# Kernel tuning notes

Hardware: AMD Instinct MI355X
Metric: run time of the kernel (lower is better)

Reference implementation:

```python
import jax, jax.numpy as jnp
import numpy as np

TIMESCALE = 10.0   # NeuralODE init kwarg
N_MAX = 48         # static upper bound on number of constant-size Dopri5 steps
B, D, H = 8192, 128, 128


def _mlp(y, W1, b1, W2, b2):
    # autonomous dynamics f(x): tanh MLP, applied along last dim
    return jnp.tanh(y @ W1 + b1) @ W2 + b2


def _dopri5_step(y, dt, f):
    # classic Dormand-Prince 5(4) tableau; autonomous f, so c_i unused
    k1 = f(y)
    k2 = f(y + dt * (1.0 / 5.0 * k1))
    k3 = f(y + dt * (3.0 / 40.0 * k1 + 9.0 / 40.0 * k2))
    k4 = f(y + dt * (44.0 / 45.0 * k1 - 56.0 / 15.0 * k2 + 32.0 / 9.0 * k3))
    k5 = f(y + dt * (19372.0 / 6561.0 * k1 - 25360.0 / 2187.0 * k2
                     + 64448.0 / 6561.0 * k3 - 212.0 / 729.0 * k4))
    k6 = f(y + dt * (9017.0 / 3168.0 * k1 - 355.0 / 33.0 * k2
                     + 46732.0 / 5247.0 * k3 + 49.0 / 176.0 * k4
                     - 5103.0 / 18656.0 * k5))
    return y + dt * (35.0 / 384.0 * k1 + 500.0 / 1113.0 * k3
                     + 125.0 / 192.0 * k4 - 2187.0 / 6784.0 * k5
                     + 11.0 / 84.0 * k6)


def _initial_step_size(y0, f0, f, order=4, rtol=1.4e-8, atol=1.4e-8):
    # faithful port of NeuralODE.initial_step_size (Hairer heuristic)
    scale = atol + jnp.abs(y0) * rtol
    d0 = jnp.linalg.norm(y0 / scale)
    d1 = jnp.linalg.norm(f0 / scale)
    h0 = jnp.where((d0 < 1e-5) | (d1 < 1e-5), 1e-6, 0.01 * d0 / d1)
    y1 = y0 + h0 * f0
    f1 = f(y1)
    d2 = jnp.linalg.norm((f1 - f0) / scale) / h0
    h1 = jnp.where((d1 <= 1e-15) & (d2 <= 1e-15),
                   jnp.maximum(1e-6, h0 * 1e-3),
                   (0.01 / (d1 + d2)) ** (1.0 / (order + 1.0)))
    return jnp.minimum(100.0 * h0, h1)


def setup_inputs() -> dict:
    key = jax.random.key(0)
    k0, k1, k2 = jax.random.split(key, 3)
    x = jax.random.normal(k0, (B, D), jnp.float32)
    W1 = jax.random.normal(k1, (D, H), jnp.float32) * (1.0 / D ** 0.5)
    b1 = jnp.zeros((H,), jnp.float32)
    W2 = jax.random.normal(k2, (H, D), jnp.float32) * (1.0 / H ** 0.5)
    b2 = jnp.zeros((D,), jnp.float32)
    t = jnp.ones((1,), jnp.float32)
    return {"t": t, "x": x, "W1": W1, "b1": b1, "W2": W2, "b2": b2}


def reference(t, x, W1, b1, W2, b2):
    f = lambda y: _mlp(y, W1, b1, W2, b2)
    # dt0 from the first state row, exactly as the original (x[0, :])
    dt0 = _initial_step_size(x[0], f(x[0]), f)
    T = t[0] / TIMESCALE  # linspace(0, t/timescale, 2) -> ts = [0, T]

    # diffrax default ConstantStepSize: fixed-dt Dopri5 until t reaches T.
    # Static-length scan with dt clamped to the remaining interval; once
    # t == T, dt == 0 and the step is skipped via lax.cond.
    step = jax.checkpoint(
        lambda y, dt: jax.lax.cond(dt > 0.0,
                                   lambda a: _dopri5_step(a, dt, f),
                                   lambda a: a, y))

    def body(carry, _):
        tt, y = carry
        dt = jnp.clip(T - tt, 0.0, dt0)
        return (tt + dt, step(y, dt)), None

    (_, yT), _ = jax.lax.scan(body, (jnp.zeros((), jnp.float32), x), None,
                              length=N_MAX)
    # SaveAt(ts=[0, T]) -> ys has leading axis n_samples=2
    return jnp.stack([x, yT])
```

## Files before the change

kernel.cpp:

```cpp
#include <hip/hip_runtime.h>


typedef __attribute__((ext_vector_type(8))) short short8;
typedef __attribute__((ext_vector_type(4))) float f32x4;

#define LDSPAD 136

__device__ __forceinline__ short f2bf(float f) {
  union { float f; unsigned u; } v; v.f = f;
  return (short)((v.u + 0x8000u) >> 16);
}

__device__ __forceinline__ float fast_tanh(float x) {
  float e = __expf(2.0f * x);
  return 1.0f - __fdividef(2.0f, e + 1.0f);
}

__global__ __launch_bounds__(256, 2)
void node_kernel(const float* __restrict__ tptr, const float* __restrict__ x,
                 const float* __restrict__ W1, const float* __restrict__ b1,
                 const float* __restrict__ W2, const float* __restrict__ b2,
                 float* __restrict__ out) {
  const int tid  = threadIdx.x;
  const int lane = tid & 63;
  const int wave = tid >> 6;
  const int q    = lane >> 4;
  const int colL = lane & 15;
  const int ctBase = wave * 2;
  const int blockRow = blockIdx.x * 16;

  __shared__ short AbufA[16][LDSPAD];
  __shared__ short AbufB[16][LDSPAD];
  __shared__ float sred[256];
  __shared__ float srowY[128], srowF[128], srowH[128], srowY2[128], srowF2[128], sscale[128];

  short8 w1f[2][4], w2f[2][4];
  float b1c[2], b2c[2];
#pragma unroll
  for (int ci = 0; ci < 2; ++ci) {
    const int n = (ctBase + ci) * 16 + colL;
    b1c[ci] = b1[n];
    b2c[ci] = b2[n];
#pragma unroll
    for (int kt = 0; kt < 4; ++kt) {
      short8 v1, v2;
#pragma unroll
      for (int j = 0; j < 8; ++j) {
        const int k = kt * 32 + q * 8 + j;
        v1[j] = f2bf(W1[k * 128 + n]);
        v2[j] = f2bf(W2[k * 128 + n]);
      }
      w1f[ci][kt] = v1;
      w2f[ci][kt] = v2;
    }
  }

  auto block_sum = [&](float v) -> float {
    sred[tid] = v;
    __syncthreads();
    if (tid < 64) {
      float s = sred[tid] + sred[tid + 64] + sred[tid + 128] + sred[tid + 192];
#pragma unroll
      for (int o = 32; o > 0; o >>= 1) s += __shfl_down(s, o, 64);
      if (tid == 0) sred[0] = s;
    }
    __syncthreads();
    float r = sred[0];
    __syncthreads();
    return r;
  };

  auto mlp_row = [&](const float* yin, float* fout) {
    if (tid < 128) {
      float a = b1[tid];
#pragma unroll 8
      for (int j = 0; j < 128; ++j) a += yin[j] * W1[j * 128 + tid];
      srowH[tid] = fast_tanh(a);
    }
    __syncthreads();
    if (tid < 128) {
      float a = b2[tid];
#pragma unroll 8
      for (int j = 0; j < 128; ++j) a += srowH[j] * W2[j * 128 + tid];
      fout[tid] = a;
    }
    __syncthreads();
  };

  if (tid < 128) srowY[tid] = x[tid];
  __syncthreads();
  mlp_row(srowY, srowF);
  float t0 = 0.f, t1 = 0.f;
  if (tid < 128) {
    float sc = 1.4e-8f + fabsf(srowY[tid]) * 1.4e-8f;
    sscale[tid] = sc;
    float a = srowY[tid] / sc; t0 = a * a;
    float bq = srowF[tid] / sc; t1 = bq * bq;
  }
  float d0 = sqrtf(block_sum(t0));
  float d1 = sqrtf(block_sum(t1));
  float h0 = (d0 < 1e-5f || d1 < 1e-5f) ? 1e-6f : 0.01f * d0 / d1;
  if (tid < 128) srowY2[tid] = srowY[tid] + h0 * srowF[tid];
  __syncthreads();
  mlp_row(srowY2, srowF2);
  float t2 = 0.f;
  if (tid < 128) { float a = (srowF2[tid] - srowF[tid]) / sscale[tid]; t2 = a * a; }
  float d2 = sqrtf(block_sum(t2)) / h0;
  float h1 = (d1 <= 1e-15f && d2 <= 1e-15f) ? fmaxf(1e-6f, h0 * 1e-3f)
                                            : powf(0.01f / (d1 + d2), 0.2f);
  const float dt0v = fminf(100.f * h0, h1);

  float yr[8];
#pragma unroll
  for (int e = 0; e < 8; ++e)
    yr[e] = x[(blockRow + q * 4 + (e & 3)) * 128 + (ctBase + (e >> 2)) * 16 + colL];

  auto stage = [&](const float* v) {
#pragma unroll
    for (int e = 0; e < 8; ++e)
      AbufA[q * 4 + (e & 3)][(ctBase + (e >> 2)) * 16 + colL] = f2bf(v[e]);
    __syncthreads();
  };

  auto evalF = [&](float* kout) {
    f32x4 accH[2];
#pragma unroll
    for (int ci = 0; ci < 2; ++ci) accH[ci] = f32x4{b1c[ci], b1c[ci], b1c[ci], b1c[ci]};
#pragma unroll
    for (int kt = 0; kt < 4; ++kt) {
      short8 a = *(const short8*)&AbufA[colL][kt * 32 + q * 8];
#pragma unroll
      for (int ci = 0; ci < 2; ++ci)
        accH[ci] = __builtin_amdgcn_mfma_f32_16x16x32_bf16(a, w1f[ci][kt], accH[ci], 0, 0, 0);
    }
#pragma unroll
    for (int e = 0; e < 8; ++e)
      AbufB[q * 4 + (e & 3)][(ctBase + (e >> 2)) * 16 + colL] =
          f2bf(fast_tanh(accH[e >> 2][e & 3]));
    __syncthreads();
    f32x4 accF[2];
#pragma unroll
    for (int ci = 0; ci < 2; ++ci) accF[ci] = f32x4{b2c[ci], b2c[ci], b2c[ci], b2c[ci]};
#pragma unroll
    for (int kt = 0; kt < 4; ++kt) {
      short8 a = *(const short8*)&AbufB[colL][kt * 32 + q * 8];
#pragma unroll
      for (int ci = 0; ci < 2; ++ci)
        accF[ci] = __builtin_amdgcn_mfma_f32_16x16x32_bf16(a, w2f[ci][kt], accF[ci], 0, 0, 0);
    }
#pragma unroll
    for (int e = 0; e < 8; ++e) kout[e] = accF[e >> 2][e & 3];
  };

  const float T = tptr[0] / 10.0f;
  float tt = 0.f;
  float k1[8], k2[8], k3[8], k4[8], k5[8], k6[8], yv[8];

#pragma unroll 1
  for (int it = 0; it < 48; ++it) {
    float dt = fminf(fmaxf(T - tt, 0.f), dt0v);
    if (dt > 0.f) {
      stage(yr); evalF(k1);
#pragma unroll
      for (int e = 0; e < 8; ++e) yv[e] = yr[e] + dt * (0.2f * k1[e]);
      stage(yv); evalF(k2);
#pragma unroll
      for (int e = 0; e < 8; ++e) yv[e] = yr[e] + dt * (0.075f * k1[e] + 0.225f * k2[e]);
      stage(yv); evalF(k3);
#pragma unroll
      for (int e = 0; e < 8; ++e)
        yv[e] = yr[e] + dt * (0.9777777777777777f * k1[e] - 3.7333333333333334f * k2[e]
                            + 3.5555555555555554f * k3[e]);
      stage(yv); evalF(k4);
#pragma unroll
      for (int e = 0; e < 8; ++e)
        yv[e] = yr[e] + dt * (2.9525986892242035f * k1[e] - 11.595793324188385f * k2[e]
                            + 9.822892851699436f * k3[e] - 0.2908093278463649f * k4[e]);
      stage(yv); evalF(k5);
#pragma unroll
      for (int e = 0; e < 8; ++e)
        yv[e] = yr[e] + dt * (2.8462752525252526f * k1[e] - 10.757575757575758f * k2[e]
                            + 8.906422717743473f * k3[e] + 0.2784090909090909f * k4[e]
                            - 0.27351165254237287f * k5[e]);
      stage(yv); evalF(k6);
#pragma unroll
      for (int e = 0; e < 8; ++e)
        yr[e] += dt * (0.0911458333333333f * k1[e] + 0.449236298292902f * k3[e]
                     + 0.6510416666666666f * k4[e] - 0.32237617924528303f * k5[e]
                     + 0.13095238095238096f * k6[e]);
    }
    tt += dt;
  }

  {
    const float4* x4 = (const float4*)(x + blockRow * 128);
    float4* o4 = (float4*)(out + blockRow * 128);
#pragma unroll 1
    for (int i = tid; i < 512; i += 256) o4[i] = x4[i];
    float* oy = out + 8192 * 128;
#pragma unroll
    for (int e = 0; e < 8; ++e)
      oy[(blockRow + q * 4 + (e & 3)) * 128 + (ctBase + (e >> 2)) * 16 + colL] = yr[e];
  }
}

extern "C" void kernel_launch(void* const* d_in, const int* in_sizes, int n_in,
                              void* d_out, int out_size, void* d_ws, size_t ws_size,
                              hipStream_t stream) {
  const float* t  = (const float*)d_in[0];
  const float* x  = (const float*)d_in[1];
  const float* W1 = (const float*)d_in[2];
  const float* b1 = (const float*)d_in[3];
  const float* W2 = (const float*)d_in[4];
  const float* b2 = (const float*)d_in[5];
  float* out = (float*)d_out;
  node_kernel<<<dim3(512), dim3(256), 0, stream>>>(t, x, W1, b1, W2, b2, out);
}
```

Baseline: 172.1 us.

## Use 8 waves per block with one column tile each and split prologue MLP

Doubles the block to 512 threads so each wave owns a single 16-column tile instead of two. This halves per-thread weight fragments and accumulators, shortening each wave's serial MFMA chain per stage. The scalar dt0 prologue MLP is split across four K-partitions with a shared-memory partial sum, replacing the single 128-thread dot-product loop. The trade-off is more waves taking part in every __syncthreads barrier and higher per-CU thread pressure at the 512-thread/4-block launch bound.

```diff
diff --git a/kernel.cpp b/kernel.cpp
--- a/kernel.cpp
+++ b/kernel.cpp
@@ -4,7 +4,7 @@
 typedef __attribute__((ext_vector_type(8))) short short8;
 typedef __attribute__((ext_vector_type(4))) float f32x4;
 
-#define LDSPAD 136
+#define SL 136
 
 __device__ __forceinline__ short f2bf(float f) {
   union { float f; unsigned u; } v; v.f = f;
@@ -16,50 +16,46 @@
   return 1.0f - __fdividef(2.0f, e + 1.0f);
 }
 
-__global__ __launch_bounds__(256, 2)
+__global__ __launch_bounds__(512, 4)
 void node_kernel(const float* __restrict__ tptr, const float* __restrict__ x,
                  const float* __restrict__ W1, const float* __restrict__ b1,
                  const float* __restrict__ W2, const float* __restrict__ b2,
                  float* __restrict__ out) {
   const int tid  = threadIdx.x;
   const int lane = tid & 63;
-  const int wave = tid >> 6;
+  const int ct   = tid >> 6;
   const int q    = lane >> 4;
   const int colL = lane & 15;
-  const int ctBase = wave * 2;
+  const int n    = ct * 16 + colL;
   const int blockRow = blockIdx.x * 16;
 
-  __shared__ short AbufA[16][LDSPAD];
-  __shared__ short AbufB[16][LDSPAD];
-  __shared__ float sred[256];
-  __shared__ float srowY[128], srowF[128], srowH[128], srowY2[128], srowF2[128], sscale[128];
+  __shared__ short A1[16][SL];
+  __shared__ short A2[16][SL];
+  __shared__ float sred[512];
+  __shared__ float spart[4][128];
+  __shared__ float srowY[128], srowH[128], srowF[128], srowY2[128], srowF2[128], sscale[128];
 
-  short8 w1f[2][4], w2f[2][4];
-  float b1c[2], b2c[2];
+  short8 w1f[4], w2f[4];
+  const float b1c = b1[n], b2c = b2[n];
 #pragma unroll
-  for (int ci = 0; ci < 2; ++ci) {
-    const int n = (ctBase + ci) * 16 + colL;
-    b1c[ci] = b1[n];
-    b2c[ci] = b2[n];
+  for (int kt = 0; kt < 4; ++kt) {
+    short8 v1, v2;
 #pragma unroll
-    for (int kt = 0; kt < 4; ++kt) {
-      short8 v1, v2;
-#pragma unroll
-      for (int j = 0; j < 8; ++j) {
-        const int k = kt * 32 + q * 8 + j;
-        v1[j] = f2bf(W1[k * 128 + n]);
-        v2[j] = f2bf(W2[k * 128 + n]);
-      }
-      w1f[ci][kt] = v1;
-      w2f[ci][kt] = v2;
+    for (int j = 0; j < 8; ++j) {
+      const int k = kt * 32 + q * 8 + j;
+      v1[j] = f2bf(W1[k * 128 + n]);
+      v2[j] = f2bf(W2[k * 128 + n]);
     }
+    w1f[kt] = v1; w2f[kt] = v2;
   }
 
   auto block_sum = [&](float v) -> float {
     sred[tid] = v;
     __syncthreads();
     if (tid < 64) {
-      float s = sred[tid] + sred[tid + 64] + sred[tid + 128] + sred[tid + 192];
+      float s = 0.f;
+#pragma unroll
+      for (int i = 0; i < 8; ++i) s += sred[tid + 64 * i];
 #pragma unroll
       for (int o = 32; o > 0; o >>= 1) s += __shfl_down(s, o, 64);
       if (tid == 0) sred[0] = s;
@@ -70,26 +66,26 @@
     return r;
   };
 
-  auto mlp_row = [&](const float* yin, float* fout) {
-    if (tid < 128) {
-      float a = b1[tid];
+  auto mlp_layer = [&](const float* vin, const float* Wg, const float* bg,
+                       float* vout, bool dotanh) {
+    const int col = tid & 127, part = tid >> 7;
+    float s = 0.f;
+    const float* wp = Wg + (part * 32) * 128 + col;
 #pragma unroll 8
-      for (int j = 0; j < 128; ++j) a += yin[j] * W1[j * 128 + tid];
-      srowH[tid] = fast_tanh(a);
-    }
+    for (int j = 0; j < 32; ++j) s += vin[part * 32 + j] * wp[j * 128];
+    spart[part][col] = s;
     __syncthreads();
     if (tid < 128) {
-      float a = b2[tid];
-#pragma unroll 8
-      for (int j = 0; j < 128; ++j) a += srowH[j] * W2[j * 128 + tid];
-      fout[tid] = a;
+      float a = bg[tid] + spart[0][tid] + spart[1][tid] + spart[2][tid] + spart[3][tid];
+      vout[tid] = dotanh ? fast_tanh(a) : a;
     }
     __syncthreads();
   };
 
   if (tid < 128) srowY[tid] = x[tid];
   __syncthreads();
-  mlp_row(srowY, srowF);
+  mlp_layer(srowY, W1, b1, srowH, true);
+  mlp_layer(srowH, W2, b2, srowF, false);
   float t0 = 0.f, t1 = 0.f;
   if (tid < 128) {
     float sc = 1.4e-8f + fabsf(srowY[tid]) * 1.4e-8f;
@@ -102,7 +98,8 @@
   float h0 = (d0 < 1e-5f || d1 < 1e-5f) ? 1e-6f : 0.01f * d0 / d1;
   if (tid < 128) srowY2[tid] = srowY[tid] + h0 * srowF[tid];
   __syncthreads();
-  mlp_row(srowY2, srowF2);
+  mlp_layer(srowY2, W1, b1, srowH, true);
+  mlp_layer(srowH, W2, b2, srowF2, false);
   float t2 = 0.f;
   if (tid < 128) { float a = (srowF2[tid] - srowF[tid]) / sscale[tid]; t2 = a * a; }
   float d2 = sqrtf(block_sum(t2)) / h0;
@@ -110,84 +107,55 @@
                                             : powf(0.01f / (d1 + d2), 0.2f);
   const float dt0v = fminf(100.f * h0, h1);
 
-  float yr[8];
+  f32x4 yr;
 #pragma unroll
-  for (int e = 0; e < 8; ++e)
-    yr[e] = x[(blockRow + q * 4 + (e & 3)) * 128 + (ctBase + (e >> 2)) * 16 + colL];
+  for (int r = 0; r < 4; ++r) yr[r] = x[(blockRow + q * 4 + r) * 128 + n];
 
-  auto stage = [&](const float* v) {
+  short* wr1 = &A1[q * 4][n];
+  short* wr2 = &A2[q * 4][n];
+  const short* rd1 = &A1[colL][q * 8];
+  const short* rd2 = &A2[colL][q * 8];
+
+  auto evalF = [&](f32x4 yin) -> f32x4 {
 #pragma unroll
-    for (int e = 0; e < 8; ++e)
-      AbufA[q * 4 + (e & 3)][(ctBase + (e >> 2)) * 16 + colL] = f2bf(v[e]);
+    for (int r = 0; r < 4; ++r) wr1[r * SL] = f2bf(yin[r]);
     __syncthreads();
-  };
-
-  auto evalF = [&](float* kout) {
-    f32x4 accH[2];
+    f32x4 acc = {b1c, b1c, b1c, b1c};
 #pragma unroll
-    for (int ci = 0; ci < 2; ++ci) accH[ci] = f32x4{b1c[ci], b1c[ci], b1c[ci], b1c[ci]};
+    for (int kt = 0; kt < 4; ++kt)
+      acc = __builtin_amdgcn_mfma_f32_16x16x32_bf16(
+          *(const short8*)(rd1 + kt * 32), w1f[kt], acc, 0, 0, 0);
 #pragma unroll
-    for (int kt = 0; kt < 4; ++kt) {
-      short8 a = *(const short8*)&AbufA[colL][kt * 32 + q * 8];
+    for (int r = 0; r < 4; ++r) wr2[r * SL] = f2bf(fast_tanh(acc[r]));
+    __syncthreads();
+    f32x4 accF = {b2c, b2c, b2c, b2c};
 #pragma unroll
-      for (int ci = 0; ci < 2; ++ci)
-        accH[ci] = __builtin_amdgcn_mfma_f32_16x16x32_bf16(a, w1f[ci][kt], accH[ci], 0, 0, 0);
-    }
-#pragma unroll
-    for (int e = 0; e < 8; ++e)
-      AbufB[q * 4 + (e & 3)][(ctBase + (e >> 2)) * 16 + colL] =
-          f2bf(fast_tanh(accH[e >> 2][e & 3]));
-    __syncthreads();
-    f32x4 accF[2];
-#pragma unroll
-    for (int ci = 0; ci < 2; ++ci) accF[ci] = f32x4{b2c[ci], b2c[ci], b2c[ci], b2c[ci]};
-#pragma unroll
-    for (int kt = 0; kt < 4; ++kt) {
-      short8 a = *(const short8*)&AbufB[colL][kt * 32 + q * 8];
-#pragma unroll
-      for (int ci = 0; ci < 2; ++ci)
-        accF[ci] = __builtin_amdgcn_mfma_f32_16x16x32_bf16(a, w2f[ci][kt], accF[ci], 0, 0, 0);
-    }
-#pragma unroll
-    for (int e = 0; e < 8; ++e) kout[e] = accF[e >> 2][e & 3];
+    for (int kt = 0; kt < 4; ++kt)
+      accF = __builtin_amdgcn_mfma_f32_16x16x32_bf16(
+          *(const short8*)(rd2 + kt * 32), w2f[kt], accF, 0, 0, 0);
+    return accF;
   };
 
   const float T = tptr[0] / 10.0f;
   float tt = 0.f;
-  float k1[8], k2[8], k3[8], k4[8], k5[8], k6[8], yv[8];
 
 #pragma unroll 1
   for (int it = 0; it < 48; ++it) {
     float dt = fminf(fmaxf(T - tt, 0.f), dt0v);
     if (dt > 0.f) {
-      stage(yr); evalF(k1);
-#pragma unroll
-      for (int e = 0; e < 8; ++e) yv[e] = yr[e] + dt * (0.2f * k1[e]);
-      stage(yv); evalF(k2);
-#pragma unroll
-      for (int e = 0; e < 8; ++e) yv[e] = yr[e] + dt * (0.075f * k1[e] + 0.225f * k2[e]);
-      stage(yv); evalF(k3);
-#pragma unroll
-      for (int e = 0; e < 8; ++e)
-        yv[e] = yr[e] + dt * (0.9777777777777777f * k1[e] - 3.7333333333333334f * k2[e]
-                            + 3.5555555555555554f * k3[e]);
-      stage(yv); evalF(k4);
-#pragma unroll
-      for (int e = 0; e < 8; ++e)
-        yv[e] = yr[e] + dt * (2.9525986892242035f * k1[e] - 11.595793324188385f * k2[e]
-                            + 9.822892851699436f * k3[e] - 0.2908093278463649f * k4[e]);
-      stage(yv); evalF(k5);
-#pragma unroll
-      for (int e = 0; e < 8; ++e)
-        yv[e] = yr[e] + dt * (2.8462752525252526f * k1[e] - 10.757575757575758f * k2[e]
-                            + 8.906422717743473f * k3[e] + 0.2784090909090909f * k4[e]
-                            - 0.27351165254237287f * k5[e]);
-      stage(yv); evalF(k6);
-#pragma unroll
-      for (int e = 0; e < 8; ++e)
-        yr[e] += dt * (0.0911458333333333f * k1[e] + 0.449236298292902f * k3[e]
-                     + 0.6510416666666666f * k4[e] - 0.32237617924528303f * k5[e]
-                     + 0.13095238095238096f * k6[e]);
+      f32x4 k1 = evalF(yr);
+      f32x4 k2 = evalF(yr + dt * (0.2f * k1));
+      f32x4 k3 = evalF(yr + dt * (0.075f * k1 + 0.225f * k2));
+      f32x4 k4 = evalF(yr + dt * (0.9777777777777777f * k1 - 3.7333333333333334f * k2
+                                + 3.5555555555555554f * k3));
+      f32x4 k5 = evalF(yr + dt * (2.9525986892242035f * k1 - 11.595793324188385f * k2
+                                + 9.822892851699436f * k3 - 0.2908093278463649f * k4));
+      f32x4 k6 = evalF(yr + dt * (2.8462752525252526f * k1 - 10.757575757575758f * k2
+                                + 8.906422717743473f * k3 + 0.2784090909090909f * k4
+                                - 0.27351165254237287f * k5));
+      yr = yr + dt * (0.0911458333333333f * k1 + 0.449236298292902f * k3
+                    + 0.6510416666666666f * k4 - 0.32237617924528303f * k5
+                    + 0.13095238095238096f * k6);
     }
     tt += dt;
   }
@@ -195,12 +163,11 @@
   {
     const float4* x4 = (const float4*)(x + blockRow * 128);
     float4* o4 = (float4*)(out + blockRow * 128);
-#pragma unroll 1
-    for (int i = tid; i < 512; i += 256) o4[i] = x4[i];
+    o4[tid] = x4[tid];
     float* oy = out + 8192 * 128;
 #pragma unroll
-    for (int e = 0; e < 8; ++e)
-      oy[(blockRow + q * 4 + (e & 3)) * 128 + (ctBase + (e >> 2)) * 16 + colL] = yr[e];
+    for (int r = 0; r < 4; ++r)
+      oy[(blockRow + q * 4 + r) * 128 + n] = yr[r];
   }
 }
 
@@ -214,5 +181,5 @@
   const float* W2 = (const float*)d_in[4];
   const float* b2 = (const float*)d_in[5];
   float* out = (float*)d_out;
-  node_kernel<<<dim3(512), dim3(256), 0, stream>>>(t, x, W1, b1, W2, b2, out);
+  node_kernel<<<dim3(512), dim3(512), 0, stream>>>(t, x, W1, b1, W2, b2, out);
 }
```

Result: faster. 168.3 us (-2.2%).
